# Kernel optimization log

Hardware: AMD Instinct MI355X
Metric: run time of the kernel (lower is better)

The kernel has to match this reference:

```python
import jax, jax.numpy as jnp
import numpy as np

N, E, C = 50000, 800000, 128
NEG_SLOPE = 0.01

def leaky(v):
    return jnp.where(v >= 0, v, NEG_SLOPE * v)

def setup_inputs() -> dict:
    key = jax.random.key(0)
    ks = jax.random.split(key, 16)
    s = lambda *sh: 1.0 / np.sqrt(sh[0])
    return {
        "x": jax.random.normal(ks[0], (N, C), dtype=jnp.float32),
        "pos": jax.random.normal(ks[1], (N, 3), dtype=jnp.float32),
        "edge_index": jax.random.randint(ks[2], (2, E), 0, N, dtype=jnp.int64),
        # mlp_h: Linear(C,C) -> LeakyReLU -> Linear(C,3) -> Tanh
        "h_w1": jax.random.uniform(ks[3], (C, C), jnp.float32, -s(C), s(C)),
        "h_b1": jax.random.uniform(ks[4], (C,), jnp.float32, -s(C), s(C)),
        "h_w2": jax.random.uniform(ks[5], (C, 3), jnp.float32, -s(C), s(C)),
        "h_b2": jax.random.uniform(ks[6], (3,), jnp.float32, -s(C), s(C)),
        # mlp_f: Linear(C+3, C) -> LeakyReLU
        "f_w": jax.random.uniform(ks[7], (C + 3, C), jnp.float32, -s(C + 3), s(C + 3)),
        "f_b": jax.random.uniform(ks[8], (C,), jnp.float32, -s(C + 3), s(C + 3)),
        # mlp_g: Linear(C,C) -> LeakyReLU -> Linear(C,C)
        "g_w1": jax.random.uniform(ks[9], (C, C), jnp.float32, -s(C), s(C)),
        "g_b1": jax.random.uniform(ks[10], (C,), jnp.float32, -s(C), s(C)),
        "g_w2": jax.random.uniform(ks[11], (C, C), jnp.float32, -s(C), s(C)),
        "g_b2": jax.random.uniform(ks[12], (C,), jnp.float32, -s(C), s(C)),
    }

def reference(x, pos, edge_index, h_w1, h_b1, h_w2, h_b2, f_w, f_b,
              g_w1, g_b1, g_w2, g_b2):
    src = edge_index[0]  # j (source)
    dst = edge_index[1]  # i (target)
    # delta_i = mlp_h(x_i): [N, 3]
    delta = jnp.tanh(leaky(x @ h_w1 + h_b1) @ h_w2 + h_b2)
    # edge message: mlp_f(cat([pos_j - pos_i + delta_i, x_j]))  -> [E, C]
    rel = pos[src] - pos[dst] + delta[dst]            # [E, 3]
    msg_in = jnp.concatenate([rel, x[src]], axis=-1)  # [E, C+3]
    e = leaky(msg_in @ f_w + f_b)                     # [E, C]
    # sum-aggregate messages at target nodes
    aggr = jax.ops.segment_sum(e, dst, num_segments=N)  # [N, C]
    # out = mlp_g(aggr) + x
    out = leaky(aggr @ g_w1 + g_b1) @ g_w2 + g_b2 + x
    return out
```

## Files before the change

### kernel.cpp

```cpp
#include <hip/hip_runtime.h>
#include <hip/hip_bf16.h>
#include <math.h>


typedef __attribute__((ext_vector_type(8))) short bf16x8;
typedef __attribute__((ext_vector_type(4))) float f32x4;

#define LEAKY(v) ((v) >= 0.0f ? (v) : 0.01f * (v))

#define KMAX 512
#define S3_BATCH 8192

static __device__ __forceinline__ unsigned short f2bf(float f) {
    unsigned u = __float_as_uint(f);
    u = (u + 0x7fffu + ((u >> 16) & 1u)) >> 16;
    return (unsigned short)u;
}

union ABu { unsigned short u[8]; bf16x8 v; };

static __device__ __forceinline__ bf16x8 cvt8(const float* __restrict__ p) {
    ABu r;
    const float4 v0 = *(const float4*)p;
    const float4 v1 = *(const float4*)(p + 4);
    r.u[0] = f2bf(v0.x); r.u[1] = f2bf(v0.y); r.u[2] = f2bf(v0.z); r.u[3] = f2bf(v0.w);
    r.u[4] = f2bf(v1.x); r.u[5] = f2bf(v1.y); r.u[6] = f2bf(v1.z); r.u[7] = f2bf(v1.w);
    return r.v;
}

static __device__ __forceinline__ bf16x8 zero_ab() {
    ABu r;
    #pragma unroll
    for (int i = 0; i < 8; ++i) r.u[i] = 0;
    return r.v;
}

static __device__ __forceinline__ void stage_weight(
    const unsigned short* __restrict__ src, unsigned short (*dst)[136], int tid)
{
    #pragma unroll
    for (int it = 0; it < 8; ++it) {
        const int c   = it * 256 + tid;
        const int row = c >> 4;
        const int col = (c & 15) * 8;
        *(uint4*)&dst[row][col] = *(const uint4*)(src + row * 128 + col);
    }
}

__global__ __launch_bounds__(128) void prep_weights(
    const float* __restrict__ h_w1, const float* __restrict__ f_w,
    const float* __restrict__ g_w1, const float* __restrict__ g_w2,
    unsigned short* __restrict__ Wht, unsigned short* __restrict__ Wft,
    unsigned short* __restrict__ G1t, unsigned short* __restrict__ G2t)
{
    const int j = blockIdx.x;
    const int k = threadIdx.x;
    Wht[j * 128 + k] = f2bf(h_w1[(size_t)k * 128 + j]);
    Wft[j * 128 + k] = f2bf(f_w[(size_t)(3 + k) * 128 + j]);
    G1t[j * 128 + k] = f2bf(g_w1[(size_t)k * 128 + j]);
    G2t[j * 128 + k] = f2bf(g_w2[(size_t)k * 128 + j]);
}

__global__ __launch_bounds__(256) void node_pre(
    const float* __restrict__ x, const float* __restrict__ pos,
    const unsigned short* __restrict__ Wht, const float* __restrict__ h_b1,
    const float* __restrict__ h_w2, const float* __restrict__ h_b2,
    const unsigned short* __restrict__ Wft, const float* __restrict__ f_b,
    const float* __restrict__ fw3,
    float* __restrict__ deltap, unsigned short* __restrict__ Zb, int N)
{
    __shared__ unsigned short Ws[128][136];
    __shared__ float cb[128][8];

    const int tid  = threadIdx.x;
    const int lane = tid & 63;
    const int wave = tid >> 6;
    const int quad = lane >> 4;
    const int l16  = lane & 15;
    const int row0 = blockIdx.x * 64 + wave * 16;

    if (tid < 128) {
        cb[tid][0] = h_b1[tid];
        cb[tid][1] = f_b[tid];
        cb[tid][2] = h_w2[tid * 3 + 0];
        cb[tid][3] = h_w2[tid * 3 + 1];
        cb[tid][4] = h_w2[tid * 3 + 2];
        cb[tid][5] = fw3[tid];
        cb[tid][6] = fw3[128 + tid];
        cb[tid][7] = fw3[256 + tid];
    }
    stage_weight(Wht, Ws, tid);

    bf16x8 a[4];
    {
        const int row = row0 + l16;
        if (row < N) {
            const float* xp = x + (size_t)row * 128 + quad * 8;
            #pragma unroll
            for (int kc = 0; kc < 4; ++kc) a[kc] = cvt8(xp + kc * 32);
        } else {
            #pragma unroll
            for (int kc = 0; kc < 4; ++kc) a[kc] = zero_ab();
        }
    }

    float px[4], py[4], pz[4];
    #pragma unroll
    for (int reg = 0; reg < 4; ++reg) {
        const int grow = row0 + quad * 4 + reg;
        const int gr = (grow < N) ? grow : 0;
        px[reg] = pos[(size_t)gr * 3 + 0];
        py[reg] = pos[(size_t)gr * 3 + 1];
        pz[reg] = pos[(size_t)gr * 3 + 2];
    }
    __syncthreads();

    f32x4 acch[8];
    #pragma unroll
    for (int nt = 0; nt < 8; ++nt) acch[nt] = (f32x4){0.f, 0.f, 0.f, 0.f};
    #pragma unroll
    for (int nt = 0; nt < 8; ++nt) {
        const unsigned short* wp = &Ws[nt * 16 + l16][quad * 8];
        #pragma unroll
        for (int kc = 0; kc < 4; ++kc) {
            const bf16x8 b = *(const bf16x8*)(wp + kc * 32);
            acch[nt] = __builtin_amdgcn_mfma_f32_16x16x32_bf16(a[kc], b, acch[nt], 0, 0, 0);
        }
    }

    __syncthreads();
    stage_weight(Wft, Ws, tid);
    __syncthreads();

    f32x4 accf[8];
    #pragma unroll
    for (int nt = 0; nt < 8; ++nt) accf[nt] = (f32x4){0.f, 0.f, 0.f, 0.f};
    #pragma unroll
    for (int nt = 0; nt < 8; ++nt) {
        const unsigned short* wp = &Ws[nt * 16 + l16][quad * 8];
        #pragma unroll
        for (int kc = 0; kc < 4; ++kc) {
            const bf16x8 b = *(const bf16x8*)(wp + kc * 32);
            accf[nt] = __builtin_amdgcn_mfma_f32_16x16x32_bf16(a[kc], b, accf[nt], 0, 0, 0);
        }
    }

    float p[4][3];
    #pragma unroll
    for (int r = 0; r < 4; ++r) { p[r][0] = 0.f; p[r][1] = 0.f; p[r][2] = 0.f; }

    #pragma unroll
    for (int nt = 0; nt < 8; ++nt) {
        const int col = nt * 16 + l16;
        const float b1  = cb[col][0];
        const float fb  = cb[col][1];
        const float w20 = cb[col][2];
        const float w21 = cb[col][3];
        const float w22 = cb[col][4];
        const float wxc = cb[col][5];
        const float wyc = cb[col][6];
        const float wzc = cb[col][7];
        #pragma unroll
        for (int reg = 0; reg < 4; ++reg) {
            const int grow = row0 + quad * 4 + reg;
            float h = acch[nt][reg] + b1;
            h = LEAKY(h);
            p[reg][0] += h * w20;
            p[reg][1] += h * w21;
            p[reg][2] += h * w22;
            if (grow < N) {
                const float z = accf[nt][reg] + fb
                              + px[reg] * wxc + py[reg] * wyc + pz[reg] * wzc;
                Zb[(size_t)grow * 128 + col] = f2bf(z);
            }
        }
    }

    #pragma unroll
    for (int reg = 0; reg < 4; ++reg)
        #pragma unroll
        for (int c = 0; c < 3; ++c) {
            float v = p[reg][c];
            v += __shfl_down(v, 8);
            v += __shfl_down(v, 4);
            v += __shfl_down(v, 2);
            v += __shfl_down(v, 1);
            p[reg][c] = v;
        }

    if (l16 == 0) {
        #pragma unroll
        for (int reg = 0; reg < 4; ++reg) {
            const int grow = row0 + quad * 4 + reg;
            if (grow < N) {
                deltap[(size_t)grow * 3 + 0] = tanhf(p[reg][0] + h_b2[0]) - px[reg];
                deltap[(size_t)grow * 3 + 1] = tanhf(p[reg][1] + h_b2[1]) - py[reg];
                deltap[(size_t)grow * 3 + 2] = tanhf(p[reg][2] + h_b2[2]) - pz[reg];
            }
        }
    }
}

__global__ __launch_bounds__(256) void coarse_hist(
    const int* __restrict__ ei, int* __restrict__ bincnt, int E, int K)
{
    __shared__ int h[KMAX];
    const int tid = threadIdx.x;
    for (int k = tid; k < K; k += 256) h[k] = 0;
    __syncthreads();
    const int stride = gridDim.x * 256;
    for (int e = blockIdx.x * 256 + tid; e < E; e += stride)
        atomicAdd(&h[ei[(size_t)E + e] >> 7], 1);
    __syncthreads();
    for (int k = tid; k < K; k += 256) {
        const int v = h[k];
        if (v) atomicAdd(&bincnt[k], v);
    }
}

__global__ __launch_bounds__(512) void bin_scan(
    const int* __restrict__ bincnt, int* __restrict__ binstart,
    int* __restrict__ cursors, int E, int K)
{
    __shared__ int s[512];
    const int tid = threadIdx.x;
    const int c = (tid < K) ? bincnt[tid] : 0;
    s[tid] = c;
    __syncthreads();
    for (int d = 1; d < 512; d <<= 1) {
        const int t = (tid >= d) ? s[tid - d] : 0;
        __syncthreads();
        s[tid] += t;
        __syncthreads();
    }
    if (tid < K) {
        binstart[tid] = s[tid] - c;
        cursors[tid]  = s[tid] - c;
    }
    if (tid == 0) binstart[K] = E;
}

__global__ __launch_bounds__(512) void binsort(
    const int* __restrict__ ei, int* __restrict__ cursors,
    unsigned int* __restrict__ binned, int E, int K)
{
    __shared__ int h[KMAX];
    __shared__ int hE[KMAX];
    __shared__ int cur[KMAX];
    __shared__ int gbase[KMAX];
    __shared__ int s[512];
    __shared__ unsigned int stage[S3_BATCH];
    __shared__ unsigned short binid[S3_BATCH];

    const int tid = threadIdx.x;
    const int e0  = blockIdx.x * S3_BATCH;
    const int m   = min(S3_BATCH, E - e0);

    for (int k = tid; k < K; k += 512) h[k] = 0;
    __syncthreads();

    #pragma unroll
    for (int j = 0; j < S3_BATCH / 512; ++j) {
        const int i = j * 512 + tid;
        if (i < m) atomicAdd(&h[ei[(size_t)E + e0 + i] >> 7], 1);
    }
    __syncthreads();

    const int c = (tid < K) ? h[tid] : 0;
    s[tid] = c;
    __syncthreads();
    for (int d = 1; d < 512; d <<= 1) {
        const int t = (tid >= d) ? s[tid - d] : 0;
        __syncthreads();
        s[tid] += t;
        __syncthreads();
    }
    if (tid < K) {
        const int ex = s[tid] - c;
        hE[tid]  = ex;
        cur[tid] = ex;
        gbase[tid] = c ? atomicAdd(&cursors[tid], c) : 0;
    }
    __syncthreads();

    #pragma unroll
    for (int j = 0; j < S3_BATCH / 512; ++j) {
        const int i = j * 512 + tid;
        if (i < m) {
            const int src = ei[e0 + i];
            const int dst = ei[(size_t)E + e0 + i];
            const int k = dst >> 7;
            const int p = atomicAdd(&cur[k], 1);
            stage[p] = (unsigned int)src | ((unsigned int)(dst & 127) << 16);
            binid[p] = (unsigned short)k;
        }
    }
    __syncthreads();

    #pragma unroll
    for (int j = 0; j < S3_BATCH / 512; ++j) {
        const int i = j * 512 + tid;
        if (i < m) {
            const int k = binid[i];
            binned[(size_t)gbase[k] + (i - hE[k])] = stage[i];
        }
    }
}

__global__ __launch_bounds__(256) void bin_finalize(
    const unsigned int* __restrict__ binned, const int* __restrict__ binstart,
    unsigned short* __restrict__ srcs_sorted,
    int* __restrict__ counts, int* __restrict__ offs_end, int N)
{
    __shared__ int h[128];
    __shared__ int s[128];
    __shared__ int cur[128];
    const int tid = threadIdx.x;
    const int b   = blockIdx.x;
    const int s0  = binstart[b];
    const int s1  = binstart[b + 1];
    const int len = s1 - s0;

    if (tid < 128) h[tid] = 0;
    __syncthreads();

    for (int i = tid; i < len; i += 256)
        atomicAdd(&h[binned[(size_t)s0 + i] >> 16], 1);
    __syncthreads();

    if (tid < 128) s[tid] = h[tid];
    __syncthreads();
    for (int d = 1; d < 128; d <<= 1) {
        int t = 0;
        if (tid < 128 && tid >= d) t = s[tid - d];
        __syncthreads();
        if (tid < 128) s[tid] += t;
        __syncthreads();
    }

    if (tid < 128) {
        const int dglob = b * 128 + tid;
        if (dglob < N) {
            counts[dglob]   = h[tid];
            offs_end[dglob] = s0 + s[tid];
        }
        cur[tid] = s0 + s[tid] - h[tid];
    }
    __syncthreads();

    for (int i = tid; i < len; i += 256) {
        const unsigned int r = binned[(size_t)s0 + i];
        const int p = atomicAdd(&cur[r >> 16], 1);
        srcs_sorted[p] = (unsigned short)(r & 0xffffu);
    }
}

__global__ __launch_bounds__(256) void aggregate_kernel(
    const unsigned short* __restrict__ srcs_sorted,
    const int* __restrict__ offs_end,
    const int* __restrict__ counts,
    const float* __restrict__ deltap,
    const unsigned short* __restrict__ Zb,
    const float* __restrict__ fw3,
    float* __restrict__ aggr,
    int N)
{
    const int lane = threadIdx.x & 63;
    const int d = blockIdx.x * 4 + (threadIdx.x >> 6);
    if (d >= N) return;

    const int quarter = lane >> 4;
    const int cl      = (lane & 15) * 8;

    const float q0 = deltap[(size_t)d * 3 + 0];
    const float q1 = deltap[(size_t)d * 3 + 1];
    const float q2 = deltap[(size_t)d * 3 + 2];

    float qd[8];
    #pragma unroll
    for (int j = 0; j < 8; ++j)
        qd[j] = q0 * fw3[cl + j] + q1 * fw3[128 + cl + j] + q2 * fw3[256 + cl + j];

    const int len   = counts[d];
    const int start = offs_end[d] - len;

    float acc[8] = {0.f, 0.f, 0.f, 0.f, 0.f, 0.f, 0.f, 0.f};

    for (int chunk = 0; chunk < len; chunk += 64) {
        const int m = min(64, len - chunk);
        int idx = 0;
        if (lane < m) idx = srcs_sorted[start + chunk + lane];

        int t = 0;
        #pragma unroll 4
        for (; t + 4 <= m; t += 4) {
            const int s = __shfl(idx, t + quarter);
            const uint4 y = *(const uint4*)(Zb + (size_t)s * 128 + cl);
            const float f0 = __uint_as_float((y.x & 0xffffu) << 16);
            const float f1 = __uint_as_float(y.x & 0xffff0000u);
            const float f2 = __uint_as_float((y.y & 0xffffu) << 16);
            const float f3 = __uint_as_float(y.y & 0xffff0000u);
            const float f4 = __uint_as_float((y.z & 0xffffu) << 16);
            const float f5 = __uint_as_float(y.z & 0xffff0000u);
            const float f6 = __uint_as_float((y.w & 0xffffu) << 16);
            const float f7 = __uint_as_float(y.w & 0xffff0000u);
            const float z0 = f0 + qd[0], z1 = f1 + qd[1];
            const float z2 = f2 + qd[2], z3 = f3 + qd[3];
            const float z4 = f4 + qd[4], z5 = f5 + qd[5];
            const float z6 = f6 + qd[6], z7 = f7 + qd[7];
            acc[0] += fmaxf(z0, 0.01f * z0);
            acc[1] += fmaxf(z1, 0.01f * z1);
            acc[2] += fmaxf(z2, 0.01f * z2);
            acc[3] += fmaxf(z3, 0.01f * z3);
            acc[4] += fmaxf(z4, 0.01f * z4);
            acc[5] += fmaxf(z5, 0.01f * z5);
            acc[6] += fmaxf(z6, 0.01f * z6);
            acc[7] += fmaxf(z7, 0.01f * z7);
        }
        if (t < m) {
            const int e = t + quarter;
            const int s = __shfl(idx, e);
            if (e < m) {
                const uint4 y = *(const uint4*)(Zb + (size_t)s * 128 + cl);
                const float f0 = __uint_as_float((y.x & 0xffffu) << 16);
                const float f1 = __uint_as_float(y.x & 0xffff0000u);
                const float f2 = __uint_as_float((y.y & 0xffffu) << 16);
                const float f3 = __uint_as_float(y.y & 0xffff0000u);
                const float f4 = __uint_as_float((y.z & 0xffffu) << 16);
                const float f5 = __uint_as_float(y.z & 0xffff0000u);
                const float f6 = __uint_as_float((y.w & 0xffffu) << 16);
                const float f7 = __uint_as_float(y.w & 0xffff0000u);
                const float z0 = f0 + qd[0], z1 = f1 + qd[1];
                const float z2 = f2 + qd[2], z3 = f3 + qd[3];
                const float z4 = f4 + qd[4], z5 = f5 + qd[5];
                const float z6 = f6 + qd[6], z7 = f7 + qd[7];
                acc[0] += fmaxf(z0, 0.01f * z0);
                acc[1] += fmaxf(z1, 0.01f * z1);
                acc[2] += fmaxf(z2, 0.01f * z2);
                acc[3] += fmaxf(z3, 0.01f * z3);
                acc[4] += fmaxf(z4, 0.01f * z4);
                acc[5] += fmaxf(z5, 0.01f * z5);
                acc[6] += fmaxf(z6, 0.01f * z6);
                acc[7] += fmaxf(z7, 0.01f * z7);
            }
        }
    }

    #pragma unroll
    for (int j = 0; j < 8; ++j) {
        acc[j] += __shfl_xor(acc[j], 16);
        acc[j] += __shfl_xor(acc[j], 32);
    }
    if (quarter == 0) {
        *(float4*)(aggr + (size_t)d * 128 + cl) =
            make_float4(acc[0], acc[1], acc[2], acc[3]);
        *(float4*)(aggr + (size_t)d * 128 + cl + 4) =
            make_float4(acc[4], acc[5], acc[6], acc[7]);
    }
}

__global__ __launch_bounds__(256) void gemm_g(
    const float* __restrict__ aggr,
    const unsigned short* __restrict__ G1t, const float* __restrict__ g_b1,
    const unsigned short* __restrict__ G2t, const float* __restrict__ g_b2,
    const float* __restrict__ x,
    float* __restrict__ out, int N)
{
    __shared__ unsigned short Ws[128][136];
    __shared__ unsigned short Ts[64][136];

    const int tid  = threadIdx.x;
    const int lane = tid & 63;
    const int wave = tid >> 6;
    const int quad = lane >> 4;
    const int l16  = lane & 15;
    const int row0 = blockIdx.x * 64 + wave * 16;

    stage_weight(G1t, Ws, tid);

    bf16x8 a[4];
    {
        const int row = row0 + l16;
        if (row < N) {
            const float* ap = aggr + (size_t)row * 128 + quad * 8;
            #pragma unroll
            for (int kc = 0; kc < 4; ++kc) a[kc] = cvt8(ap + kc * 32);
        } else {
            #pragma unroll
            for (int kc = 0; kc < 4; ++kc) a[kc] = zero_ab();
        }
    }
    __syncthreads();

    f32x4 acc[8];
    #pragma unroll
    for (int nt = 0; nt < 8; ++nt) acc[nt] = (f32x4){0.f, 0.f, 0.f, 0.f};
    #pragma unroll
    for (int nt = 0; nt < 8; ++nt) {
        const unsigned short* wp = &Ws[nt * 16 + l16][quad * 8];
        #pragma unroll
        for (int kc = 0; kc < 4; ++kc) {
            const bf16x8 b = *(const bf16x8*)(wp + kc * 32);
            acc[nt] = __builtin_amdgcn_mfma_f32_16x16x32_bf16(a[kc], b, acc[nt], 0, 0, 0);
        }
    }

    #pragma unroll
    for (int nt = 0; nt < 8; ++nt) {
        const int col = nt * 16 + l16;
        const float b1 = g_b1[col];
        #pragma unroll
        for (int reg = 0; reg < 4; ++reg) {
            float t = acc[nt][reg] + b1;
            t = LEAKY(t);
            Ts[wave * 16 + quad * 4 + reg][col] = f2bf(t);
        }
    }
    __syncthreads();
    stage_weight(G2t, Ws, tid);
    __syncthreads();

    bf16x8 a2[4];
    {
        const unsigned short* tp = &Ts[wave * 16 + l16][quad * 8];
        #pragma unroll
        for (int kc = 0; kc < 4; ++kc) a2[kc] = *(const bf16x8*)(tp + kc * 32);
    }

    f32x4 acc2[8];
    #pragma unroll
    for (int nt = 0; nt < 8; ++nt) acc2[nt] = (f32x4){0.f, 0.f, 0.f, 0.f};
    #pragma unroll
    for (int nt = 0; nt < 8; ++nt) {
        const unsigned short* wp = &Ws[nt * 16 + l16][quad * 8];
        #pragma unroll
        for (int kc = 0; kc < 4; ++kc) {
            const bf16x8 b = *(const bf16x8*)(wp + kc * 32);
            acc2[nt] = __builtin_amdgcn_mfma_f32_16x16x32_bf16(a2[kc], b, acc2[nt], 0, 0, 0);
        }
    }

    #pragma unroll
    for (int nt = 0; nt < 8; ++nt) {
        const int col = nt * 16 + l16;
        const float b2 = g_b2[col];
        #pragma unroll
        for (int reg = 0; reg < 4; ++reg) {
            const int grow = row0 + quad * 4 + reg;
            if (grow < N)
                out[(size_t)grow * 128 + col] =
                    acc2[nt][reg] + b2 + x[(size_t)grow * 128 + col];
        }
    }
}

extern "C" void kernel_launch(void* const* d_in, const int* in_sizes, int n_in,
                              void* d_out, int out_size, void* d_ws, size_t ws_size,
                              hipStream_t stream) {
    const float* x    = (const float*)d_in[0];
    const float* pos  = (const float*)d_in[1];
    const int*   ei   = (const int*)d_in[2];
    const float* h_w1 = (const float*)d_in[3];
    const float* h_b1 = (const float*)d_in[4];
    const float* h_w2 = (const float*)d_in[5];
    const float* h_b2 = (const float*)d_in[6];
    const float* f_w  = (const float*)d_in[7];
    const float* f_b  = (const float*)d_in[8];
    const float* g_w1 = (const float*)d_in[9];
    const float* g_b1 = (const float*)d_in[10];
    const float* g_w2 = (const float*)d_in[11];
    const float* g_b2 = (const float*)d_in[12];
    float* out = (float*)d_out;

    const int N = in_sizes[0] / 128;
    const int E = in_sizes[2] / 2;
    const int K = (N + 127) >> 7;

    float* deltap         = (float*)d_ws;
    unsigned short* Zb    = (unsigned short*)(deltap + (size_t)N * 3);
    int* counts           = (int*)(Zb + (size_t)N * 128);
    int* offs_end         = counts + N;
    int* bincnt           = offs_end + N;
    int* binstart         = bincnt + KMAX;
    int* cursors          = binstart + (KMAX + 1);
    unsigned short* srcs  = (unsigned short*)(cursors + KMAX + 1);
    unsigned int* binned  = (unsigned int*)(srcs + (((size_t)E + 1) & ~(size_t)1));
    unsigned short* Wht   = (unsigned short*)(binned + E);
    unsigned short* Wft   = Wht + 128 * 128;
    unsigned short* G1t   = Wft + 128 * 128;
    unsigned short* G2t   = G1t + 128 * 128;
    float* aggr           = out;

    const int tile_blocks = (N + 63) / 64;
    const int sort_blocks = (E + S3_BATCH - 1) / S3_BATCH;

    hipMemsetAsync(bincnt, 0, KMAX * sizeof(int), stream);

    prep_weights<<<128, 128, 0, stream>>>(h_w1, f_w, g_w1, g_w2, Wht, Wft, G1t, G2t);

    coarse_hist<<<128, 256, 0, stream>>>(ei, bincnt, E, K);
    bin_scan<<<1, 512, 0, stream>>>(bincnt, binstart, cursors, E, K);

    node_pre<<<tile_blocks, 256, 0, stream>>>(x, pos, Wht, h_b1, h_w2, h_b2, Wft, f_b,
                                              f_w, deltap, Zb, N);

    binsort<<<sort_blocks, 512, 0, stream>>>(ei, cursors, binned, E, K);
    bin_finalize<<<K, 256, 0, stream>>>(binned, binstart, srcs, counts, offs_end, N);

    aggregate_kernel<<<(N + 3) / 4, 256, 0, stream>>>(
        srcs, offs_end, counts, deltap, Zb, f_w, aggr, N);

    gemm_g<<<tile_blocks, 256, 0, stream>>>(aggr, G1t, g_b1, G2t, g_b2, x, out, N);
}
```

Measured before the change: 227.7 us.

## Fuse histogram scan into last block, drop memset, bf16 aggregate buffer, wider binsort

The zeroing of the bin counters moves into prep_weights, which removes the separate memset. The single-block scan is fused into coarse_hist using a last-block-done atomic counter, cutting two launches. binsort now uses 1024-thread blocks. aggregate_kernel writes the aggregated features as bf16 into a workspace buffer instead of fp32 into out, which halves the traffic between it and gemm_g. The last-block pattern relies on threadfence ordering and an extra done counter that must be reset on every call.

```diff
diff --git a/kernel.cpp b/kernel.cpp
--- a/kernel.cpp
+++ b/kernel.cpp
@@ -51,10 +51,15 @@
     const float* __restrict__ h_w1, const float* __restrict__ f_w,
     const float* __restrict__ g_w1, const float* __restrict__ g_w2,
     unsigned short* __restrict__ Wht, unsigned short* __restrict__ Wft,
-    unsigned short* __restrict__ G1t, unsigned short* __restrict__ G2t)
+    unsigned short* __restrict__ G1t, unsigned short* __restrict__ G2t,
+    int* __restrict__ bincnt, int* __restrict__ done)
 {
     const int j = blockIdx.x;
     const int k = threadIdx.x;
+    if (j == 0) {
+        for (int i = k; i < KMAX; i += 128) bincnt[i] = 0;
+        if (k == 0) *done = 0;
+    }
     Wht[j * 128 + k] = f2bf(h_w1[(size_t)k * 128 + j]);
     Wft[j * 128 + k] = f2bf(f_w[(size_t)(3 + k) * 128 + j]);
     G1t[j * 128 + k] = f2bf(g_w1[(size_t)k * 128 + j]);
@@ -201,30 +206,32 @@
     }
 }
 
-__global__ __launch_bounds__(256) void coarse_hist(
-    const int* __restrict__ ei, int* __restrict__ bincnt, int E, int K)
+__global__ __launch_bounds__(512) void coarse_hist(
+    const int* __restrict__ ei, int* __restrict__ bincnt,
+    int* __restrict__ binstart, int* __restrict__ cursors,
+    int* __restrict__ done, int E, int K)
 {
     __shared__ int h[KMAX];
+    __shared__ int s[512];
+    __shared__ int lastflag;
     const int tid = threadIdx.x;
-    for (int k = tid; k < K; k += 256) h[k] = 0;
-    __syncthreads();
-    const int stride = gridDim.x * 256;
-    for (int e = blockIdx.x * 256 + tid; e < E; e += stride)
+    for (int k = tid; k < K; k += 512) h[k] = 0;
+    __syncthreads();
+    const int stride = gridDim.x * 512;
+    for (int e = blockIdx.x * 512 + tid; e < E; e += stride)
         atomicAdd(&h[ei[(size_t)E + e] >> 7], 1);
     __syncthreads();
-    for (int k = tid; k < K; k += 256) {
+    for (int k = tid; k < K; k += 512) {
         const int v = h[k];
         if (v) atomicAdd(&bincnt[k], v);
     }
-}
-
-__global__ __launch_bounds__(512) void bin_scan(
-    const int* __restrict__ bincnt, int* __restrict__ binstart,
-    int* __restrict__ cursors, int E, int K)
-{
-    __shared__ int s[512];
-    const int tid = threadIdx.x;
-    const int c = (tid < K) ? bincnt[tid] : 0;
+    __threadfence();
+    __syncthreads();
+    if (tid == 0) lastflag = (atomicAdd(done, 1) == (int)gridDim.x - 1) ? 1 : 0;
+    __syncthreads();
+    if (!lastflag) return;
+
+    const int c = (tid < K) ? atomicAdd(&bincnt[tid], 0) : 0;
     s[tid] = c;
     __syncthreads();
     for (int d = 1; d < 512; d <<= 1) {
@@ -240,7 +247,7 @@
     if (tid == 0) binstart[K] = E;
 }
 
-__global__ __launch_bounds__(512) void binsort(
+__global__ __launch_bounds__(1024) void binsort(
     const int* __restrict__ ei, int* __restrict__ cursors,
     unsigned int* __restrict__ binned, int E, int K)
 {
@@ -256,23 +263,27 @@
     const int e0  = blockIdx.x * S3_BATCH;
     const int m   = min(S3_BATCH, E - e0);
 
-    for (int k = tid; k < K; k += 512) h[k] = 0;
-    __syncthreads();
-
-    #pragma unroll
-    for (int j = 0; j < S3_BATCH / 512; ++j) {
-        const int i = j * 512 + tid;
+    for (int k = tid; k < K; k += 1024) h[k] = 0;
+    __syncthreads();
+
+    #pragma unroll
+    for (int j = 0; j < S3_BATCH / 1024; ++j) {
+        const int i = j * 1024 + tid;
         if (i < m) atomicAdd(&h[ei[(size_t)E + e0 + i] >> 7], 1);
     }
     __syncthreads();
 
-    const int c = (tid < K) ? h[tid] : 0;
-    s[tid] = c;
+    int c = 0;
+    if (tid < 512) {
+        c = (tid < K) ? h[tid] : 0;
+        s[tid] = c;
+    }
     __syncthreads();
     for (int d = 1; d < 512; d <<= 1) {
-        const int t = (tid >= d) ? s[tid - d] : 0;
+        int t = 0;
+        if (tid < 512 && tid >= d) t = s[tid - d];
         __syncthreads();
-        s[tid] += t;
+        if (tid < 512) s[tid] += t;
         __syncthreads();
     }
     if (tid < K) {
@@ -284,8 +295,8 @@
     __syncthreads();
 
     #pragma unroll
-    for (int j = 0; j < S3_BATCH / 512; ++j) {
-        const int i = j * 512 + tid;
+    for (int j = 0; j < S3_BATCH / 1024; ++j) {
+        const int i = j * 1024 + tid;
         if (i < m) {
             const int src = ei[e0 + i];
             const int dst = ei[(size_t)E + e0 + i];
@@ -298,8 +309,8 @@
     __syncthreads();
 
     #pragma unroll
-    for (int j = 0; j < S3_BATCH / 512; ++j) {
-        const int i = j * 512 + tid;
+    for (int j = 0; j < S3_BATCH / 1024; ++j) {
+        const int i = j * 1024 + tid;
         if (i < m) {
             const int k = binid[i];
             binned[(size_t)gbase[k] + (i - hE[k])] = stage[i];
@@ -362,7 +373,7 @@
     const float* __restrict__ deltap,
     const unsigned short* __restrict__ Zb,
     const float* __restrict__ fw3,
-    float* __restrict__ aggr,
+    unsigned short* __restrict__ Ab,
     int N)
 {
     const int lane = threadIdx.x & 63;
@@ -452,15 +463,15 @@
         acc[j] += __shfl_xor(acc[j], 32);
     }
     if (quarter == 0) {
-        *(float4*)(aggr + (size_t)d * 128 + cl) =
-            make_float4(acc[0], acc[1], acc[2], acc[3]);
-        *(float4*)(aggr + (size_t)d * 128 + cl + 4) =
-            make_float4(acc[4], acc[5], acc[6], acc[7]);
+        ABu o;
+        #pragma unroll
+        for (int j = 0; j < 8; ++j) o.u[j] = f2bf(acc[j]);
+        *(bf16x8*)(Ab + (size_t)d * 128 + cl) = o.v;
     }
 }
 
 __global__ __launch_bounds__(256) void gemm_g(
-    const float* __restrict__ aggr,
+    const unsigned short* __restrict__ Ab,
     const unsigned short* __restrict__ G1t, const float* __restrict__ g_b1,
     const unsigned short* __restrict__ G2t, const float* __restrict__ g_b2,
     const float* __restrict__ x,
@@ -482,9 +493,9 @@
     {
         const int row = row0 + l16;
         if (row < N) {
-            const float* ap = aggr + (size_t)row * 128 + quad * 8;
+            const unsigned short* ap = Ab + (size_t)row * 128 + quad * 8;
             #pragma unroll
-            for (int kc = 0; kc < 4; ++kc) a[kc] = cvt8(ap + kc * 32);
+            for (int kc = 0; kc < 4; ++kc) a[kc] = *(const bf16x8*)(ap + kc * 32);
         } else {
             #pragma unroll
             for (int kc = 0; kc < 4; ++kc) a[kc] = zero_ab();
@@ -583,32 +594,31 @@
     int* bincnt           = offs_end + N;
     int* binstart         = bincnt + KMAX;
     int* cursors          = binstart + (KMAX + 1);
-    unsigned short* srcs  = (unsigned short*)(cursors + KMAX + 1);
+    int* done             = cursors + KMAX;
+    unsigned short* srcs  = (unsigned short*)(done + 1);
     unsigned int* binned  = (unsigned int*)(srcs + (((size_t)E + 1) & ~(size_t)1));
     unsigned short* Wht   = (unsigned short*)(binned + E);
     unsigned short* Wft   = Wht + 128 * 128;
     unsigned short* G1t   = Wft + 128 * 128;
     unsigned short* G2t   = G1t + 128 * 128;
-    float* aggr           = out;
+    unsigned short* Ab    = G2t + 128 * 128;
 
     const int tile_blocks = (N + 63) / 64;
     const int sort_blocks = (E + S3_BATCH - 1) / S3_BATCH;
 
-    hipMemsetAsync(bincnt, 0, KMAX * sizeof(int), stream);
-
-    prep_weights<<<128, 128, 0, stream>>>(h_w1, f_w, g_w1, g_w2, Wht, Wft, G1t, G2t);
-
-    coarse_hist<<<128, 256, 0, stream>>>(ei, bincnt, E, K);
-    bin_scan<<<1, 512, 0, stream>>>(bincnt, binstart, cursors, E, K);
+    prep_weights<<<128, 128, 0, stream>>>(h_w1, f_w, g_w1, g_w2, Wht, Wft, G1t, G2t,
+                                          bincnt, done);
+
+    coarse_hist<<<128, 512, 0, stream>>>(ei, bincnt, binstart, cursors, done, E, K);
 
     node_pre<<<tile_blocks, 256, 0, stream>>>(x, pos, Wht, h_b1, h_w2, h_b2, Wft, f_b,
                                               f_w, deltap, Zb, N);
 
-    binsort<<<sort_blocks, 512, 0, stream>>>(ei, cursors, binned, E, K);
+    binsort<<<sort_blocks, 1024, 0, stream>>>(ei, cursors, binned, E, K);
     bin_finalize<<<K, 256, 0, stream>>>(binned, binstart, srcs, counts, offs_end, N);
 
     aggregate_kernel<<<(N + 3) / 4, 256, 0, stream>>>(
-        srcs, offs_end, counts, deltap, Zb, f_w, aggr, N);
-
-    gemm_g<<<tile_blocks, 256, 0, stream>>>(aggr, G1t, g_b1, G2t, g_b2, x, out, N);
-}
+        srcs, offs_end, counts, deltap, Zb, f_w, Ab, N);
+
+    gemm_g<<<tile_blocks, 256, 0, stream>>>(Ab, G1t, g_b1, G2t, g_b2, x, out, N);
+}
```

Result: no change. 226.5 us (-0.5%).
